# Kernel optimization log

Hardware: AMD Instinct MI355X
Metric: run time of the kernel (lower is better)

The kernel has to match this reference:

```python
import jax, jax.numpy as jnp
import numpy as np
from jax import lax

B, IN_C, DIM, HEADS, K = 8, 64, 128, 4, 3
H, W = 96, 96
HEAD_DIM = DIM // HEADS
SCALE = HEAD_DIM ** -0.5
EPS = 1e-5  # BatchNorm eps (eval mode, running_mean=0, running_var=1)


def _conv3x3(x, w):
    return lax.conv_general_dilated(x, w, (1, 1), ((1, 1), (1, 1)),
                                    dimension_numbers=('NCHW', 'OIHW', 'NCHW'))


def _cbr(x, w, g, b):
    y = _conv3x3(x, w)
    y = y * (g / jnp.sqrt(1.0 + EPS))[None, :, None, None] + b[None, :, None, None]
    return jax.nn.relu(y)


def setup_inputs() -> dict:
    key = jax.random.key(0)
    ks = jax.random.split(key, 24)
    n = lambda i, s, sc=0.05: jax.random.normal(ks[i], s, jnp.float32) * sc
    u = lambda i, s: jax.random.uniform(ks[i], s, jnp.float32, 0.5, 1.5)
    return dict(
        x=jax.random.normal(ks[0], (B, IN_C, H, W), jnp.float32),
        fg=jax.random.normal(ks[1], (B, DIM, H, W), jnp.float32),
        conv1_w=n(2, (DIM, IN_C, 3, 3)), bn1_g=u(3, (DIM,)), bn1_b=n(4, (DIM,)),
        conv2_w=n(5, (DIM, DIM, 3, 3)), bn2_g=u(6, (DIM,)), bn2_b=n(7, (DIM,)),
        v_w=n(8, (DIM, DIM)), v_b=n(9, (DIM,)),
        attn_w=n(10, (K ** 4 * HEADS, DIM)), attn_b=n(11, (K ** 4 * HEADS,)),
        proj_w=n(12, (DIM, DIM)), proj_b=n(13, (DIM,)),
        conv3_w=n(14, (DIM, DIM, 3, 3)), bn3_g=u(15, (DIM,)), bn3_b=n(16, (DIM,)),
        conv4_w=n(17, (DIM, DIM, 3, 3)), bn4_g=u(18, (DIM,)), bn4_b=n(19, (DIM,)),
    )


def reference(x, fg, conv1_w, bn1_g, bn1_b, conv2_w, bn2_g, bn2_b,
              v_w, v_b, attn_w, attn_b, proj_w, proj_b,
              conv3_w, bn3_g, bn3_b, conv4_w, bn4_g, bn4_b):
    L = H * W
    # input_cbr: two conv3x3 + BN(eval) + ReLU
    xf = _cbr(_cbr(x, conv1_w, bn1_g, bn1_b), conv2_w, bn2_g, bn2_b)  # (B,DIM,H,W)
    xh = xf.transpose(0, 2, 3, 1)                 # (B,H,W,DIM)
    fgh = fg.transpose(0, 2, 3, 1)                # (B,H,W,DIM)
    # value projection then unfold (im2col, channel-major patch ordering like torch)
    v = (xh @ v_w.T + v_b).transpose(0, 3, 1, 2)  # (B,DIM,H,W)
    patches = lax.conv_general_dilated_patches(v, (K, K), (1, 1), ((1, 1), (1, 1)))  # (B,DIM*9,H,W)
    vp = patches.reshape(B, HEADS, HEAD_DIM, K * K, L).transpose(0, 1, 4, 3, 2)  # (B,h,L,9,hd)
    # attention logits directly from fg (stride=1 -> AvgPool identity)
    attn = (fgh @ attn_w.T + attn_b).reshape(B, L, HEADS, K * K, K * K)
    attn = attn.transpose(0, 2, 1, 3, 4) * SCALE  # (B,h,L,9,9)
    attn = jax.nn.softmax(attn, axis=-1)
    # batched small matmuls: (9,9) @ (9,hd) per window
    xw = jnp.einsum('bhlpq,bhlqd->bhlpd', attn, vp)  # (B,h,L,9,hd)
    xw = xw.transpose(0, 1, 4, 3, 2).reshape(B, DIM, K, K, H, W)  # channel-major, then (kh,kw)
    # fold: overlapping scatter-add back to (H,W)
    canvas = jnp.zeros((B, DIM, H + 2, W + 2), xw.dtype)
    for ki in range(K):
        for kj in range(K):
            canvas = canvas.at[:, :, ki:ki + H, kj:kj + W].add(xw[:, :, ki, kj])
    folded = canvas[:, :, 1:H + 1, 1:W + 1]        # crop padding
    p = (folded.transpose(0, 2, 3, 1) @ proj_w.T + proj_b).transpose(0, 3, 1, 2)
    # output_cbr
    out = _cbr(_cbr(p, conv3_w, bn3_g, bn3_b), conv4_w, bn4_g, bn4_b)
    return out
```

## Files before the change

kernel.cpp:

```cpp
#include <hip/hip_runtime.h>
#include <math.h>

typedef __attribute__((ext_vector_type(8))) short short8;
typedef __attribute__((ext_vector_type(4))) float f32x4;
typedef unsigned short u16;
typedef unsigned int u32;

#define HW   96
#define LPIX 9216
static constexpr float kScale = 0.17677669529663687f;

__device__ inline u16 f2bf(float f) {
    u32 x = __float_as_uint(f);
    return (u16)((x + 0x7fffu + ((x >> 16) & 1u)) >> 16);
}
__device__ inline float bf2f(u16 v) { return __uint_as_float((u32)v << 16); }

typedef __attribute__((address_space(1))) const void gas_t;
typedef __attribute__((address_space(3))) void las_t;
__device__ __forceinline__ void g2lds16(const void* g, void* l) {
    __builtin_amdgcn_global_load_lds((gas_t*)g, (las_t*)l, 16, 0, 0);
}

#define WAITV(n) do {                                                   \
        asm volatile("s_waitcnt vmcnt(" #n ")" ::: "memory");           \
        __builtin_amdgcn_sched_barrier(0);                              \
    } while (0)
#define SFENCE() __builtin_amdgcn_sched_barrier(0)

__global__ __launch_bounds__(256) void cast_nchw_nhwc_all(
    const float* __restrict__ x, const float* __restrict__ fg,
    u16* __restrict__ xb, u16* __restrict__ fgb)
{
    const int y = blockIdx.x, b = blockIdx.y, tid = threadIdx.x;
    const int isfg = blockIdx.z;
    const float* in = isfg ? fg : x;
    u16* out = isfg ? fgb : xb;
    const int C = isfg ? 128 : 64;

    __shared__ float sT[HW * 128];
    for (int i = tid; i < HW * C; i += 256) {
        int c = i / HW, xx = i - c * HW;
        sT[xx * C + c] = in[(((size_t)b * C + c) * HW + y) * HW + xx];
    }
    __syncthreads();
    for (int i = tid; i < HW * (C / 8); i += 256) {
        int c8 = i % (C / 8), xx = i / (C / 8);
        union { short8 v8; u16 u[8]; } pk;
#pragma unroll
        for (int j = 0; j < 8; ++j) pk.u[j] = f2bf(sT[xx * C + c8 * 8 + j]);
        *(short8*)&out[(((size_t)b * HW + y) * HW + xx) * C + c8 * 8] = pk.v8;
    }
}

__device__ __forceinline__ void conv_w_elem(
    const float* __restrict__ w, u16* __restrict__ wp, int CIN, int i)
{
    int e  = i & 7;
    int gr = i >> 3;
    int c  = gr / 4608;
    int gi = gr - c * 4608;
    int f  = gi >> 9;
    int rr = gi & 511;
    int ch = rr >> 8;
    int m  = (rr >> 2) & 63;
    int s  = rr & 3;
    int qq = (s - (m >> 1)) & 3;
    int co = ch * 64 + m;
    int ci = c * 32 + qq * 8 + e;
    wp[i] = f2bf(w[(size_t)(co * CIN + ci) * 9 + f]);
}

__device__ __forceinline__ void attn_w_elem(
    const float* __restrict__ aw, u16* __restrict__ wp, int i)
{
    int e = i & 7;
    int g = i >> 3;
    int h = g / 1536, r = g - h * 1536;
    int c4 = r / 384, r2 = r - c4 * 384;
    int rr = r2 >> 2, s = r2 & 3;
    int qq = (s - (rr >> 1)) & 3;
    int ci = c4 * 32 + qq * 8 + e;
    float v = (rr < 81) ? aw[(size_t)(h * 81 + rr) * 128 + ci] : 0.f;
    wp[i] = f2bf(v);
}

__global__ __launch_bounds__(256) void cast_weights_all(
    const float* __restrict__ c1w, const float* __restrict__ c2w,
    const float* __restrict__ c3w, const float* __restrict__ c4w,
    const float* __restrict__ vw,  const float* __restrict__ pw,
    const float* __restrict__ aw,
    u16* __restrict__ w1p, u16* __restrict__ w2p,
    u16* __restrict__ w3p, u16* __restrict__ w4p,
    u16* __restrict__ vwp, u16* __restrict__ pwp, u16* __restrict__ awp)
{
    int i = blockIdx.x * 256 + threadIdx.x;
    if (i < 73728)  { conv_w_elem(c1w, w1p, 64, i);  return; }
    i -= 73728;
    if (i < 147456) { conv_w_elem(c2w, w2p, 128, i); return; }
    i -= 147456;
    if (i < 147456) { conv_w_elem(c3w, w3p, 128, i); return; }
    i -= 147456;
    if (i < 147456) { conv_w_elem(c4w, w4p, 128, i); return; }
    i -= 147456;
    if (i < 16384)  { vwp[i] = f2bf(vw[i]); return; }
    i -= 16384;
    if (i < 16384)  { pwp[i] = f2bf(pw[i]); return; }
    i -= 16384;
    attn_w_elem(aw, awp, i);
}

template <int CIN, bool OUT_F32>
__global__ __launch_bounds__(768, 1) void conv_gemm(
    const u16* __restrict__ in, const u16* __restrict__ wp,
    const float* __restrict__ g, const float* __restrict__ be, void* outv)
{
    constexpr int NC   = CIN / 32;
    constexpr int WBYT = 73728;
    constexpr int HBYT = 36864;

    const int bx = blockIdx.x;
    const int b  = blockIdx.y;
    const int y0 = bx * 3;
    const int l0 = y0 * 96;

    const int tid = threadIdx.x, lane = tid & 63, wv = tid >> 6;
    const int half = wv & 1, ch = (wv >> 1) & 1, r = wv >> 2;
    const int lx = lane & 15, q = lane >> 4;

    __shared__ __align__(16) char smem[WBYT + 2 * HBYT];
    float* sT = (float*)smem;
    float* sF = (float*)smem;

    const int aoff = lx * 64 + (((q + (lx >> 1)) & 3) << 4);
    const int pb   = r * 96 + half * 48 + lx;

    f32x4 acc[4][3];
#pragma unroll
    for (int mt = 0; mt < 4; ++mt)
#pragma unroll
        for (int nt = 0; nt < 3; ++nt) acc[mt][nt] = (f32x4){0.f, 0.f, 0.f, 0.f};

    const u16* inb = in + (size_t)b * LPIX * CIN;

    auto STAGE_W = [&](int c) {
#pragma unroll
        for (int j = 0; j < 6; ++j) {
            g2lds16(&wp[((size_t)c * 4608 + j * 768 + tid) * 8],
                    (char*)smem + (j * 768 + wv * 64) * 16);
        }
    };
    auto STAGE_H = [&](int c, int buf) {
#pragma unroll
        for (int i = 0; i < 3; ++i) {
            int gi = i * 768 + tid;
            int p  = gi >> 2, s = gi & 3;
            int qq = (s - (p >> 1)) & 3;
            int lh = l0 - 96 + p;
            lh = lh < 0 ? 0 : (lh >= LPIX ? LPIX - 1 : lh);
            g2lds16(&inb[(size_t)lh * CIN + c * 32 + qq * 8],
                    (char*)smem + WBYT + buf * HBYT + (i * 768 + wv * 64) * 16);
        }
    };
    auto TAP = [&](int f, int hbuf) {
        const int dy = f / 3 - 1, dx = f % 3 - 1;
        const int off = dy * 96 + dx + 96;
        const bool vy = (unsigned)(y0 + r + dy) < 96u;
        const char* hb = (const char*)smem + WBYT + hbuf * HBYT;
        short8 af[4], bfr[3];
#pragma unroll
        for (int mt = 0; mt < 4; ++mt)
            af[mt] = *(const short8*)((const char*)smem + (f * 2 + ch) * 4096
                                      + mt * 1024 + aoff);
#pragma unroll
        for (int nt = 0; nt < 3; ++nt) {
            int pm = pb + nt * 16 + off;
            int slot = (q + (pm >> 1)) & 3;
            short8 t8 = *(const short8*)(hb + pm * 64 + slot * 16);
            bool ok = vy & ((unsigned)(half * 48 + nt * 16 + lx + dx) < 96u);
            bfr[nt] = ok ? t8 : (short8){0, 0, 0, 0, 0, 0, 0, 0};
        }
#pragma unroll
        for (int mt = 0; mt < 4; ++mt)
#pragma unroll
            for (int nt = 0; nt < 3; ++nt)
                acc[mt][nt] = __builtin_amdgcn_mfma_f32_16x16x32_bf16(
                    af[mt], bfr[nt], acc[mt][nt], 0, 0, 0);
    };

    STAGE_H(0, 0);
    SFENCE();
    STAGE_W(0);
    SFENCE();
    STAGE_H(1, 1);
    SFENCE();
    WAITV(3);
    __builtin_amdgcn_s_barrier();
    asm volatile("" ::: "memory");

#pragma unroll
    for (int c = 0; c < NC; ++c) {
        const int hbuf = c & 1;
        TAP(0, hbuf); TAP(1, hbuf); TAP(2, hbuf);
        TAP(3, hbuf); TAP(4, hbuf); TAP(5, hbuf);
        TAP(6, hbuf); TAP(7, hbuf); TAP(8, hbuf);
        if (c + 1 < NC) {
            asm volatile("s_waitcnt lgkmcnt(0)" ::: "memory");
            __builtin_amdgcn_s_barrier();
            asm volatile("" ::: "memory");
            STAGE_W(c + 1);
            SFENCE();
            if (c + 2 < NC) STAGE_H(c + 2, c & 1);
            SFENCE();
            if (c + 2 < NC) { WAITV(3); } else { WAITV(0); }
            __builtin_amdgcn_s_barrier();
            asm volatile("" ::: "memory");
        }
    }

    asm volatile("s_waitcnt lgkmcnt(0) vmcnt(0)" ::: "memory");
    __builtin_amdgcn_s_barrier();
    asm volatile("" ::: "memory");

    const float rs = rsqrtf(1.f + 1e-5f);
    if (OUT_F32) {
        float* out = (float*)outv;
#pragma unroll
        for (int hh = 0; hh < 2; ++hh) {
            if (hh) { __syncthreads(); }
            if (half == hh) {
#pragma unroll
                for (int mt = 0; mt < 4; ++mt)
#pragma unroll
                    for (int nt = 0; nt < 3; ++nt)
#pragma unroll
                        for (int reg = 0; reg < 4; ++reg)
                            sF[(ch * 64 + mt * 16 + q * 4 + reg) * 148
                               + r * 48 + nt * 16 + lx] = acc[mt][nt][reg];
            }
            __syncthreads();
            for (int i = tid; i < 4608; i += 768) {
                int co = i / 36, r2 = i - co * 36;
                int wrr = r2 / 12, j = r2 - wrr * 12;
                float sc = g[co] * rs, bb = be[co];
                f32x4 vv = *(const f32x4*)&sF[co * 148 + wrr * 48 + j * 4];
#pragma unroll
                for (int e = 0; e < 4; ++e) vv[e] = fmaxf(fmaf(vv[e], sc, bb), 0.f);
                *(f32x4*)&out[((size_t)b * 128 + co) * LPIX
                              + (y0 + wrr) * 96 + hh * 48 + j * 4] = vv;
            }
            if (!hh) __syncthreads();
        }
    } else {
        u16* out = (u16*)outv;
#pragma unroll
        for (int hh = 0; hh < 2; ++hh) {
            if (hh) { __syncthreads(); }
            if (half == hh) {
#pragma unroll
                for (int mt = 0; mt < 4; ++mt)
#pragma unroll
                    for (int nt = 0; nt < 3; ++nt)
#pragma unroll
                        for (int reg = 0; reg < 4; ++reg)
                            sT[(r * 48 + nt * 16 + lx) * 130
                               + ch * 64 + mt * 16 + q * 4 + reg] = acc[mt][nt][reg];
            }
            __syncthreads();
            for (int i = tid; i < 2304; i += 768) {
                int cog = i & 15, pxl = i >> 4;
                int wrr = pxl / 48, ofs = pxl - wrr * 48;
                int l = (y0 + wrr) * 96 + hh * 48 + ofs;
                union { short8 v8; u16 u[8]; } pk;
#pragma unroll
                for (int j = 0; j < 8; ++j) {
                    int co = cog * 8 + j;
                    pk.u[j] = f2bf(fmaxf(fmaf(sT[pxl * 130 + cog * 8 + j],
                                              g[co] * rs, be[co]), 0.f));
                }
                *(short8*)&out[((size_t)b * LPIX + l) * 128 + cog * 8] = pk.v8;
            }
            if (!hh) __syncthreads();
        }
    }
}

__global__ __launch_bounds__(256) void linear_mfma(
    const u16* __restrict__ in, const u16* __restrict__ wp,
    const float* __restrict__ bias, u16* __restrict__ out)
{
    const int l0 = blockIdx.x * 64;
    const int tid = threadIdx.x, lane = tid & 63, wv = tid >> 6;
    const int wm = wv >> 1, wn = wv & 1;
    const int lx = lane & 15, q = lane >> 4;

    __shared__ char smem[4 * 64 * 40 * 2 + 4 * 128 * 40 * 2];
    u16* sX = (u16*)smem;
    u16* sW = (u16*)(smem + 4 * 64 * 40 * 2);
    float* sT = (float*)smem;

    for (int i = tid; i < 1024; i += 256) {
        int k8 = i & 15, px = i >> 4;
        short8 v = *(const short8*)&in[((size_t)(l0 + px)) * 128 + k8 * 8];
        *(short8*)&sX[((k8 >> 2) * 64 + px) * 40 + (k8 & 3) * 8] = v;
    }
    for (int i = tid; i < 2048; i += 256) {
        int k8 = i & 15, co = i >> 4;
        short8 v = *(const short8*)&wp[(size_t)co * 128 + k8 * 8];
        *(short8*)&sW[((k8 >> 2) * 128 + co) * 40 + (k8 & 3) * 8] = v;
    }
    __syncthreads();

    f32x4 acc[4][2];
#pragma unroll
    for (int mt = 0; mt < 4; ++mt)
#pragma unroll
        for (int nt = 0; nt < 2; ++nt) acc[mt][nt] = (f32x4){0.f, 0.f, 0.f, 0.f};

#pragma unroll
    for (int c4 = 0; c4 < 4; ++c4) {
        short8 af[4], bfr[2];
#pragma unroll
        for (int mt = 0; mt < 4; ++mt)
            af[mt] = *(const short8*)&sW[(c4 * 128 + wm * 64 + mt * 16 + lx) * 40 + q * 8];
#pragma unroll
        for (int nt = 0; nt < 2; ++nt)
            bfr[nt] = *(const short8*)&sX[(c4 * 64 + wn * 32 + nt * 16 + lx) * 40 + q * 8];
#pragma unroll
        for (int mt = 0; mt < 4; ++mt)
#pragma unroll
            for (int nt = 0; nt < 2; ++nt)
                acc[mt][nt] = __builtin_amdgcn_mfma_f32_16x16x32_bf16(
                    af[mt], bfr[nt], acc[mt][nt], 0, 0, 0);
    }

    for (int mh = 0; mh < 2; ++mh) {
        __syncthreads();
        if (wm == mh) {
#pragma unroll
            for (int mt = 0; mt < 4; ++mt)
#pragma unroll
                for (int nt = 0; nt < 2; ++nt)
#pragma unroll
                    for (int reg = 0; reg < 4; ++reg)
                        sT[(wn * 32 + nt * 16 + lx) * 65 + mt * 16 + q * 4 + reg] =
                            acc[mt][nt][reg];
        }
        __syncthreads();
        for (int i = tid; i < 512; i += 256) {
            int cog = i & 7, px = i >> 3;
            union { short8 v8; u16 u[8]; } pk;
#pragma unroll
            for (int j = 0; j < 8; ++j) {
                int co = mh * 64 + cog * 8 + j;
                pk.u[j] = f2bf(sT[px * 65 + cog * 8 + j] + bias[co]);
            }
            *(short8*)&out[((size_t)(l0 + px)) * 128 + mh * 64 + cog * 8] = pk.v8;
        }
    }
}

__global__ __launch_bounds__(256, 2) void attn_mfma(
    const u16* __restrict__ fgb, const u16* __restrict__ awp,
    const float* __restrict__ ab, u16* __restrict__ A)
{
    const int lt = blockIdx.x, h = blockIdx.y, b = blockIdx.z;
    const int l0 = lt * 128;
    const int tid = threadIdx.x, lane = tid & 63, wv = tid >> 6;
    const int lx = lane & 15, q = lane >> 4;

    __shared__ __align__(16) char smem[57344];
    float* sL = (float*)smem;

    const u16* fb = fgb + ((size_t)b * LPIX + l0) * 128;
#pragma unroll
    for (int i = 0; i < 8; ++i) {
        int gg = i * 256 + tid;
        int c4 = gg >> 9, r = gg & 511, px = r >> 2, s = r & 3;
        int qq = (s - (px >> 1)) & 3;
        g2lds16(&fb[(size_t)px * 128 + c4 * 32 + qq * 8],
                (char*)smem + (i * 256 + wv * 64) * 16);
    }
    const u16* wb = awp + (size_t)h * 1536 * 8;
#pragma unroll
    for (int i = 0; i < 6; ++i) {
        g2lds16(&wb[(size_t)(i * 256 + tid) * 8],
                (char*)smem + 32768 + (i * 256 + wv * 64) * 16);
    }
    asm volatile("s_waitcnt vmcnt(0)" ::: "memory");
    __builtin_amdgcn_s_barrier();
    asm volatile("" ::: "memory");

    f32x4 acc[2][6];
#pragma unroll
    for (int nt = 0; nt < 2; ++nt)
#pragma unroll
        for (int j = 0; j < 6; ++j) acc[nt][j] = (f32x4){0.f, 0.f, 0.f, 0.f};

#pragma unroll
    for (int c4 = 0; c4 < 4; ++c4) {
        short8 af[2], bfr[6];
#pragma unroll
        for (int nt = 0; nt < 2; ++nt) {
            int px = wv * 32 + nt * 16 + lx;
            af[nt] = *(const short8*)((const char*)smem + c4 * 8192 + px * 64
                                      + (((q + (px >> 1)) & 3) << 4));
        }
#pragma unroll
        for (int j = 0; j < 6; ++j) {
            int rr = j * 16 + lx;
            bfr[j] = *(const short8*)((const char*)smem + 32768 + c4 * 6144 + rr * 64
                                      + (((q + (rr >> 1)) & 3) << 4));
        }
#pragma unroll
        for (int nt = 0; nt < 2; ++nt)
#pragma unroll
            for (int j = 0; j < 6; ++j)
                acc[nt][j] = __builtin_amdgcn_mfma_f32_16x16x32_bf16(
                    af[nt], bfr[j], acc[nt][j], 0, 0, 0);
    }

    __syncthreads();
#pragma unroll
    for (int nt = 0; nt < 2; ++nt)
#pragma unroll
        for (int j = 0; j < 6; ++j)
#pragma unroll
            for (int reg = 0; reg < 4; ++reg)
                sL[(wv * 32 + nt * 16 + q * 4 + reg) * 97 + j * 16 + lx] =
                    acc[nt][j][reg];
    __syncthreads();

    for (int t = tid; t < 1152; t += 256) {
        int px = t & 127, p = t >> 7;
        const int rbase = h * 81 + p * 9;
        float lg[9], m = -1e30f;
#pragma unroll
        for (int qq = 0; qq < 9; ++qq) {
            lg[qq] = (sL[px * 97 + p * 9 + qq] + ab[rbase + qq]) * kScale;
            m = fmaxf(m, lg[qq]);
        }
        float s = 0.f;
#pragma unroll
        for (int qq = 0; qq < 9; ++qq) { lg[qq] = __expf(lg[qq] - m); s += lg[qq]; }
        float inv = 1.f / s;
        u16* Ab = &A[(((size_t)(b * 4 + h) * 9 + p) * 9) * LPIX + l0 + px];
#pragma unroll
        for (int qq = 0; qq < 9; ++qq) Ab[(size_t)qq * LPIX] = f2bf(lg[qq] * inv);
    }
}

__global__ __launch_bounds__(384, 4) void attn_fold(
    const u16* __restrict__ A, const u16* __restrict__ v,
    u16* __restrict__ out)
{
    const int yt = blockIdx.x, h = blockIdx.y, b = blockIdx.z;
    const int y0 = yt * 4;
    const int tid = threadIdx.x;
    const int yl  = tid / 96;
    const int x   = tid - yl * 96;
    const int y   = y0 + yl;
    const int l   = y * 96 + x;

    __shared__ u16 sV[8 * 96 * 32];

    const u16* vb = v + (size_t)b * LPIX * 128 + h * 32;
    for (int t = tid; t < 3072; t += 384) {
        int k = t & 3, s = t >> 2;
        int r = s / 96, xx = s - r * 96;
        int gy = y0 - 2 + r;
        uint4 uu = make_uint4(0u, 0u, 0u, 0u);
        if ((unsigned)gy < 96u)
            uu = *(const uint4*)&vb[(size_t)(gy * 96 + xx) * 128 + k * 8];
        *(uint4*)&sV[(size_t)s * 32 + k * 8] = uu;
    }

    float S[25];
#pragma unroll
    for (int i = 0; i < 25; ++i) S[i] = 0.f;

    const u16* Ab = A + ((size_t)(b * 4 + h) * 81) * (size_t)LPIX;
#pragma unroll
    for (int ki = 0; ki < 3; ++ki) {
        const int ly = y + 1 - ki;
        const bool vy = ((unsigned)ly < 96u);
#pragma unroll
        for (int kj = 0; kj < 3; ++kj) {
            const int lx2 = x + 1 - kj;
            if (vy && (unsigned)lx2 < 96u) {
                const u16* Ap = Ab + (size_t)(ki * 3 + kj) * 9 * (size_t)LPIX
                              + (ly * 96 + lx2);
#pragma unroll
                for (int qq = 0; qq < 9; ++qq) {
                    const int qi = qq / 3, qj = qq - qi * 3;
                    S[(qi - ki + 2) * 5 + (qj - kj + 2)] += bf2f(Ap[(size_t)qq * LPIX]);
                }
            }
        }
    }

    __syncthreads();

    float acc[32];
#pragma unroll
    for (int c = 0; c < 32; ++c) acc[c] = 0.f;

#pragma unroll
    for (int oy = 0; oy < 5; ++oy) {
        const int r = yl + oy;
#pragma unroll
        for (int ox = 0; ox < 5; ++ox) {
            const int xx = x + ox - 2;
            if ((unsigned)xx >= 96u) continue;
            const float sc = S[oy * 5 + ox];
            const u16* vp = &sV[(size_t)(r * 96 + xx) * 32];
#pragma unroll
            for (int c8 = 0; c8 < 4; ++c8) {
                const uint4 uu = *(const uint4*)&vp[c8 * 8];
                acc[c8 * 8 + 0] = fmaf(sc, __uint_as_float(uu.x << 16),          acc[c8 * 8 + 0]);
                acc[c8 * 8 + 1] = fmaf(sc, __uint_as_float(uu.x & 0xffff0000u), acc[c8 * 8 + 1]);
                acc[c8 * 8 + 2] = fmaf(sc, __uint_as_float(uu.y << 16),          acc[c8 * 8 + 2]);
                acc[c8 * 8 + 3] = fmaf(sc, __uint_as_float(uu.y & 0xffff0000u), acc[c8 * 8 + 3]);
                acc[c8 * 8 + 4] = fmaf(sc, __uint_as_float(uu.z << 16),          acc[c8 * 8 + 4]);
                acc[c8 * 8 + 5] = fmaf(sc, __uint_as_float(uu.z & 0xffff0000u), acc[c8 * 8 + 5]);
                acc[c8 * 8 + 6] = fmaf(sc, __uint_as_float(uu.w << 16),          acc[c8 * 8 + 6]);
                acc[c8 * 8 + 7] = fmaf(sc, __uint_as_float(uu.w & 0xffff0000u), acc[c8 * 8 + 7]);
            }
        }
    }

    u16* ob = &out[((size_t)b * LPIX + l) * 128 + h * 32];
#pragma unroll
    for (int gidx = 0; gidx < 4; ++gidx) {
        union { short8 v8; u16 u[8]; } pk;
#pragma unroll
        for (int j = 0; j < 8; ++j) pk.u[j] = f2bf(acc[gidx * 8 + j]);
        *(short8*)&ob[gidx * 8] = pk.v8;
    }
}

extern "C" void kernel_launch(void* const* d_in, const int* in_sizes, int n_in,
                              void* d_out, int out_size, void* d_ws, size_t ws_size,
                              hipStream_t stream)
{
    const float* x    = (const float*)d_in[0];
    const float* fg   = (const float*)d_in[1];
    const float* c1w  = (const float*)d_in[2];
    const float* bn1g = (const float*)d_in[3];
    const float* bn1b = (const float*)d_in[4];
    const float* c2w  = (const float*)d_in[5];
    const float* bn2g = (const float*)d_in[6];
    const float* bn2b = (const float*)d_in[7];
    const float* vw   = (const float*)d_in[8];
    const float* vb   = (const float*)d_in[9];
    const float* aw   = (const float*)d_in[10];
    const float* abv  = (const float*)d_in[11];
    const float* pw   = (const float*)d_in[12];
    const float* pb   = (const float*)d_in[13];
    const float* c3w  = (const float*)d_in[14];
    const float* bn3g = (const float*)d_in[15];
    const float* bn3b = (const float*)d_in[16];
    const float* c4w  = (const float*)d_in[17];
    const float* bn4g = (const float*)d_in[18];
    const float* bn4b = (const float*)d_in[19];

    char* wsp = (char*)d_ws;
    size_t off = 0;
    auto carve = [&](size_t bytes) {
        void* pp = wsp + off;
        off += (bytes + 255) & ~(size_t)255;
        return pp;
    };
    u16*   xb   = (u16*)carve((size_t)8 * LPIX * 64 * 2);
    u16*   fgb  = (u16*)carve((size_t)8 * LPIX * 128 * 2);
    u16*   actA = (u16*)carve((size_t)8 * LPIX * 128 * 2);
    u16*   actB = (u16*)carve((size_t)8 * LPIX * 128 * 2);
    u16*   Abuf = (u16*)carve((size_t)8 * 324 * LPIX * 2);
    u16*   w1p  = (u16*)carve((size_t)9 * 2 * 128 * 32 * 2);
    u16*   w2p  = (u16*)carve((size_t)9 * 4 * 128 * 32 * 2);
    u16*   w3p  = (u16*)carve((size_t)9 * 4 * 128 * 32 * 2);
    u16*   w4p  = (u16*)carve((size_t)9 * 4 * 128 * 32 * 2);
    u16*   vwp  = (u16*)carve((size_t)128 * 128 * 2);
    u16*   pwp  = (u16*)carve((size_t)128 * 128 * 2);
    u16*   awp  = (u16*)carve((size_t)4 * 1536 * 8 * 2);

    cast_nchw_nhwc_all<<<dim3(HW, 8, 2), 256, 0, stream>>>(x, fg, xb, fgb);
    cast_weights_all<<<2336, 256, 0, stream>>>(c1w, c2w, c3w, c4w, vw, pw, aw,
                                               w1p, w2p, w3p, w4p, vwp, pwp, awp);

    conv_gemm<64, false><<<dim3(32, 8), 768, 0, stream>>>(xb, w1p, bn1g, bn1b, actA);
    conv_gemm<128, false><<<dim3(32, 8), 768, 0, stream>>>(actA, w2p, bn2g, bn2b, actB);
    linear_mfma<<<1152, 256, 0, stream>>>(actB, vwp, vb, actA);
    attn_mfma<<<dim3(72, 4, 8), 256, 0, stream>>>(fgb, awp, abv, Abuf);
    attn_fold<<<dim3(24, 4, 8), 384, 0, stream>>>(Abuf, actA, actB);
    linear_mfma<<<1152, 256, 0, stream>>>(actB, pwp, pb, actA);
    conv_gemm<128, false><<<dim3(32, 8), 768, 0, stream>>>(actA, w3p, bn3g, bn3b, actB);
    conv_gemm<128, true><<<dim3(32, 8), 768, 0, stream>>>(actB, w4p, bn4g, bn4b, d_out);
}
```

Before: 350.9 us.

## Fold proj linear into conv3 weights with border-aware bias correction

Precomposes the projection linear layer into the conv3 weights (W3·Pw) and drops the separate proj linear_mfma launch. The projection bias passes through the zero-padded conv as a per-tap sum, so it is added as a per-channel table in the conv3 epilogue with edge and corner corrections. This removes one full read/write pass over the activation tensor and one kernel launch. In exchange, weight preprocessing now does a 128-long dot product per element, and bf16 rounding of the fused weights changes numerics slightly.

```diff
diff --git a/kernel.cpp b/kernel.cpp
--- a/kernel.cpp
+++ b/kernel.cpp
@@ -53,21 +53,29 @@
     }
 }
 
-__device__ __forceinline__ void conv_w_elem(
-    const float* __restrict__ w, u16* __restrict__ wp, int CIN, int i)
+__device__ __forceinline__ void conv_w_decode(
+    int i, int CIN, int& co, int& ci, int& f)
 {
     int e  = i & 7;
     int gr = i >> 3;
     int c  = gr / 4608;
     int gi = gr - c * 4608;
-    int f  = gi >> 9;
+    f  = gi >> 9;
     int rr = gi & 511;
     int ch = rr >> 8;
     int m  = (rr >> 2) & 63;
     int s  = rr & 3;
     int qq = (s - (m >> 1)) & 3;
-    int co = ch * 64 + m;
-    int ci = c * 32 + qq * 8 + e;
+    co = ch * 64 + m;
+    ci = c * 32 + qq * 8 + e;
+    (void)CIN;
+}
+
+__device__ __forceinline__ void conv_w_elem(
+    const float* __restrict__ w, u16* __restrict__ wp, int CIN, int i)
+{
+    int co, ci, f;
+    conv_w_decode(i, CIN, co, ci, f);
     wp[i] = f2bf(w[(size_t)(co * CIN + ci) * 9 + f]);
 }
 
@@ -88,32 +96,67 @@
 __global__ __launch_bounds__(256) void cast_weights_all(
     const float* __restrict__ c1w, const float* __restrict__ c2w,
     const float* __restrict__ c3w, const float* __restrict__ c4w,
-    const float* __restrict__ vw,  const float* __restrict__ pw,
-    const float* __restrict__ aw,
+    const float* __restrict__ vw,  const float* __restrict__ aw,
+    const float* __restrict__ pw,  const float* __restrict__ pb,
     u16* __restrict__ w1p, u16* __restrict__ w2p,
     u16* __restrict__ w3p, u16* __restrict__ w4p,
-    u16* __restrict__ vwp, u16* __restrict__ pwp, u16* __restrict__ awp)
+    u16* __restrict__ vwp, u16* __restrict__ awp,
+    float* __restrict__ bt)
 {
     int i = blockIdx.x * 256 + threadIdx.x;
     if (i < 73728)  { conv_w_elem(c1w, w1p, 64, i);  return; }
     i -= 73728;
     if (i < 147456) { conv_w_elem(c2w, w2p, 128, i); return; }
     i -= 147456;
-    if (i < 147456) { conv_w_elem(c3w, w3p, 128, i); return; }
+    if (i < 147456) {
+        int co, k, f;
+        conv_w_decode(i, 128, co, k, f);
+        float acc = 0.f;
+#pragma unroll 4
+        for (int ci3 = 0; ci3 < 128; ++ci3)
+            acc = fmaf(c3w[(size_t)(co * 128 + ci3) * 9 + f], pw[ci3 * 128 + k], acc);
+        w3p[i] = f2bf(acc);
+        return;
+    }
     i -= 147456;
     if (i < 147456) { conv_w_elem(c4w, w4p, 128, i); return; }
     i -= 147456;
     if (i < 16384)  { vwp[i] = f2bf(vw[i]); return; }
     i -= 16384;
-    if (i < 16384)  { pwp[i] = f2bf(pw[i]); return; }
-    i -= 16384;
-    attn_w_elem(aw, awp, i);
-}
-
-template <int CIN, bool OUT_F32>
+    if (i < 49152)  { attn_w_elem(aw, awp, i); return; }
+    i -= 49152;
+    if (i >= 1152) return;
+    {
+        int t = i >> 7, co = i & 127;
+        float bf9[9];
+#pragma unroll
+        for (int f = 0; f < 9; ++f) {
+            float a = 0.f;
+            for (int ci3 = 0; ci3 < 128; ++ci3)
+                a = fmaf(c3w[(size_t)(co * 128 + ci3) * 9 + f], pb[ci3], a);
+            bf9[f] = a;
+        }
+        float v;
+        switch (t) {
+            case 0: v = bf9[0]+bf9[1]+bf9[2]+bf9[3]+bf9[4]+bf9[5]+bf9[6]+bf9[7]+bf9[8]; break;
+            case 1: v = bf9[0]+bf9[1]+bf9[2]; break;
+            case 2: v = bf9[6]+bf9[7]+bf9[8]; break;
+            case 3: v = bf9[0]+bf9[3]+bf9[6]; break;
+            case 4: v = bf9[2]+bf9[5]+bf9[8]; break;
+            case 5: v = bf9[0]; break;
+            case 6: v = bf9[2]; break;
+            case 7: v = bf9[6]; break;
+            default: v = bf9[8]; break;
+        }
+        bt[t * 128 + co] = v;
+    }
+}
+
+template <int CIN, bool OUT_F32, bool PBC>
 __global__ __launch_bounds__(768, 1) void conv_gemm(
     const u16* __restrict__ in, const u16* __restrict__ wp,
-    const float* __restrict__ g, const float* __restrict__ be, void* outv)
+    const float* __restrict__ g, const float* __restrict__ be,
+    const float* __restrict__ bt, void* outv)
 {
     constexpr int NC   = CIN / 32;
     constexpr int WBYT = 73728;
@@ -270,13 +313,31 @@
             for (int i = tid; i < 2304; i += 768) {
                 int cog = i & 15, pxl = i >> 4;
                 int wrr = pxl / 48, ofs = pxl - wrr * 48;
-                int l = (y0 + wrr) * 96 + hh * 48 + ofs;
+                int yy = y0 + wrr, xc = hh * 48 + ofs;
+                int l = yy * 96 + xc;
+                bool top = false, bot = false, lft = false, rgt = false;
+                if (PBC) {
+                    top = (yy == 0); bot = (yy == 95);
+                    lft = (xc == 0); rgt = (xc == 95);
+                }
                 union { short8 v8; u16 u[8]; } pk;
 #pragma unroll
                 for (int j = 0; j < 8; ++j) {
                     int co = cog * 8 + j;
-                    pk.u[j] = f2bf(fmaxf(fmaf(sT[pxl * 130 + cog * 8 + j],
-                                              g[co] * rs, be[co]), 0.f));
+                    float val = sT[pxl * 130 + cog * 8 + j];
+                    if (PBC) {
+                        float corr = bt[co];
+                        if (top) corr -= bt[128 + co];
+                        if (bot) corr -= bt[256 + co];
+                        if (lft) corr -= bt[384 + co];
+                        if (rgt) corr -= bt[512 + co];
+                        if (top && lft) corr += bt[640 + co];
+                        if (top && rgt) corr += bt[768 + co];
+                        if (bot && lft) corr += bt[896 + co];
+                        if (bot && rgt) corr += bt[1024 + co];
+                        val += corr;
+                    }
+                    pk.u[j] = f2bf(fmaxf(fmaf(val, g[co] * rs, be[co]), 0.f));
                 }
                 *(short8*)&out[((size_t)b * LPIX + l) * 128 + cog * 8] = pk.v8;
             }
@@ -581,19 +642,18 @@
     u16*   w3p  = (u16*)carve((size_t)9 * 4 * 128 * 32 * 2);
     u16*   w4p  = (u16*)carve((size_t)9 * 4 * 128 * 32 * 2);
     u16*   vwp  = (u16*)carve((size_t)128 * 128 * 2);
-    u16*   pwp  = (u16*)carve((size_t)128 * 128 * 2);
     u16*   awp  = (u16*)carve((size_t)4 * 1536 * 8 * 2);
+    float* btab = (float*)carve((size_t)9 * 128 * 4);
 
     cast_nchw_nhwc_all<<<dim3(HW, 8, 2), 256, 0, stream>>>(x, fg, xb, fgb);
-    cast_weights_all<<<2336, 256, 0, stream>>>(c1w, c2w, c3w, c4w, vw, pw, aw,
-                                               w1p, w2p, w3p, w4p, vwp, pwp, awp);
-
-    conv_gemm<64, false><<<dim3(32, 8), 768, 0, stream>>>(xb, w1p, bn1g, bn1b, actA);
-    conv_gemm<128, false><<<dim3(32, 8), 768, 0, stream>>>(actA, w2p, bn2g, bn2b, actB);
+    cast_weights_all<<<2277, 256, 0, stream>>>(c1w, c2w, c3w, c4w, vw, aw, pw, pb,
+                                               w1p, w2p, w3p, w4p, vwp, awp, btab);
+
+    conv_gemm<64, false, false><<<dim3(32, 8), 768, 0, stream>>>(xb, w1p, bn1g, bn1b, nullptr, actA);
+    conv_gemm<128, false, false><<<dim3(32, 8), 768, 0, stream>>>(actA, w2p, bn2g, bn2b, nullptr, actB);
     linear_mfma<<<1152, 256, 0, stream>>>(actB, vwp, vb, actA);
     attn_mfma<<<dim3(72, 4, 8), 256, 0, stream>>>(fgb, awp, abv, Abuf);
     attn_fold<<<dim3(24, 4, 8), 384, 0, stream>>>(Abuf, actA, actB);
-    linear_mfma<<<1152, 256, 0, stream>>>(actB, pwp, pb, actA);
-    conv_gemm<128, false><<<dim3(32, 8), 768, 0, stream>>>(actA, w3p, bn3g, bn3b, actB);
-    conv_gemm<128, true><<<dim3(32, 8), 768, 0, stream>>>(actB, w4p, bn4g, bn4b, d_out);
-}
+    conv_gemm<128, false, true><<<dim3(32, 8), 768, 0, stream>>>(actB, w3p, bn3g, bn3b, btab, actA);
+    conv_gemm<128, true, false><<<dim3(32, 8), 768, 0, stream>>>(actA, w4p, bn4g, bn4b, nullptr, d_out);
+}
```

New measurement: 479.4 us. 36.6% more time.
